# Optimization experiments

Hardware: AMD Instinct MI355X
Metric: run time of the kernel (lower is better)

Reference implementation:

```python
import jax, jax.numpy as jnp
import numpy as np

B, S, D = 4, 4096, 1024   # batch, seq_len, d_model
E, K, H = 8, 2, 2048      # num_experts, top_k, expert hidden dim


def setup_inputs() -> dict:
    key = jax.random.key(0)
    k0, k1, k2, k3, k4 = jax.random.split(key, 5)
    scale = 0.02
    return {
        "x": jax.random.normal(k0, (B, S, D), jnp.float32),
        "gate_w": jax.random.normal(k1, (D, E), jnp.float32) * scale,      # nn.Linear(d_model, E, bias=False)
        "w_gate": jax.random.normal(k2, (E, D, H), jnp.float32) * scale,   # expert SwiGLU gate proj
        "w_up":   jax.random.normal(k3, (E, D, H), jnp.float32) * scale,   # expert up proj
        "w_down": jax.random.normal(k4, (E, H, D), jnp.float32) * scale,   # expert down proj
    }


def reference(x, gate_w, w_gate, w_up, w_down):
    b, s, d = x.shape
    e = gate_w.shape[1]
    x_flat = x.reshape(-1, d)                          # [T, D], T = B*S

    gate_logits = x_flat @ gate_w                      # [T, E] (eval mode: no noise)
    top_logits, top_idx = jax.lax.top_k(gate_logits, K)  # [T, K]
    top_w = jax.nn.softmax(top_logits.astype(jnp.float32), axis=1).astype(x.dtype)  # [T, K]

    # load-balancing aux loss (Switch/Mixtral style)
    f_i = jax.nn.one_hot(top_idx, e, dtype=jnp.float32).sum(axis=1).mean(axis=0)  # [E]
    p_i = jax.nn.softmax(gate_logits, axis=1).mean(axis=0)                        # [E]
    aux_loss = (f_i * p_i).sum() * (e ** 2)

    flat_idx = top_idx.reshape(-1)                     # [T*K] expert ids
    # pre-scale token copies by routing weight (matches original)
    y = (x_flat[:, None, :] * top_w[:, :, None]).reshape(-1, d)  # [T*K, D]

    expert_out = jnp.zeros_like(y)
    for i in range(e):  # fixed small expert count: dense-fallback masked MLP
        h = jax.nn.silu(y @ w_gate[i]) * (y @ w_up[i])           # [T*K, H]
        o_i = h @ w_down[i]                                      # [T*K, D]
        expert_out = jnp.where((flat_idx == i)[:, None], o_i, expert_out)

    # faithful to original: scatter_add indexed by EXPERT id (as written in source)
    final = jnp.zeros_like(x_flat).at[flat_idx].add(expert_out)  # [T, D]
    return final.reshape(b, s, d), aux_loss
```

## Files before the change

kernel.cpp:

```cpp
#include <hip/hip_runtime.h>
#include <hip/hip_bf16.h>
#include <stdint.h>

#define T_TOK  16384
#define DMODEL 1024
#define NEXP   8
#define HDIM   2048
#define CAPSL  16512

#define BM 128
#define BN 128
#define NWORK_MAX 264
#define YROWS_MAX (NWORK_MAX*BM)
#define GRID_GEMM (NWORK_MAX * 16)

#define OFF_COUNTS 0
#define OFF_NWORK  64
#define OFF_FSUM   128
#define OFF_PSUM   192
#define OFF_WORK   256
#define OFF_HSUM   8192
#define OFF_ZERO_END 73728
#define OFF_TOK    131072
#define OFF_WGT    786432
#define OFF_WT     2097152
#define WT_ELEMS   (NEXP*HDIM*DMODEL)
#define OFF_Y      (OFF_WT + (size_t)2*WT_ELEMS*2)
#define NEED_FAST  (OFF_Y + (size_t)YROWS_MAX*DMODEL*2)

typedef __attribute__((ext_vector_type(4))) float f32x4;
typedef __attribute__((ext_vector_type(8))) short bf16x8;

__device__ __forceinline__ unsigned short f2bf(float f) {
    unsigned int u = __builtin_bit_cast(unsigned int, f);
    unsigned int r = (u + 0x7fffu + ((u >> 16) & 1u)) >> 16;
    return (unsigned short)r;
}

__global__ __launch_bounds__(256) void wt_fragment(const float* __restrict__ wg,
                                                   const float* __restrict__ wu,
                                                   unsigned short* __restrict__ wt_out) {
    int mat = blockIdx.z;
    const float* src = mat ? wu : wg;
    unsigned short* dst = wt_out + (size_t)mat * WT_ELEMS;
    int e  = blockIdx.y;
    int kt = blockIdx.x & 15;
    int ht = blockIdx.x >> 4;
    __shared__ unsigned short tile[64][68];
    const float* s = src + ((size_t)e * DMODEL + kt * 64) * HDIM + ht * 64;
    for (int u = threadIdx.x; u < 1024; u += 256) {
        int r = u >> 4, c = (u & 15) * 4;
        float4 v = *(const float4*)(s + (size_t)r * HDIM + c);
        tile[r][c + 0] = f2bf(v.x); tile[r][c + 1] = f2bf(v.y);
        tile[r][c + 2] = f2bf(v.z); tile[r][c + 3] = f2bf(v.w);
    }
    __syncthreads();
    for (int cc = threadIdx.x; cc < 512; cc += 256) {
        int r   = cc & 15;
        int q   = (cc >> 4) & 3;
        int sl  = (cc >> 6) & 1;
        int ntl = cc >> 7;
        int hh  = ntl * 16 + r;
        int ddb = sl * 32 + q * 8;
        bf16x8 o;
        #pragma unroll
        for (int j = 0; j < 8; ++j) o[j] = (short)tile[ddb + j][hh];
        size_t idx = ((((size_t)e * 128 + ht * 4 + ntl) * 32 + kt * 2 + sl) * 4 + q) * 128
                     + r * 8;
        *(bf16x8*)(dst + idx) = o;
    }
}

__global__ __launch_bounds__(256) void gating(const float* __restrict__ x,
                                              const float* __restrict__ gw,
                                              int* counts, float* fsum, float* psum,
                                              int* tok_list, float* wgt_list) {
    __shared__ float gws_t[NEXP * DMODEL];
    __shared__ int   ch_e[64][2];
    __shared__ float ch_w[64][2];
    __shared__ float pacc[NEXP];
    __shared__ int   hist[NEXP], gbase[NEXP], cursor[NEXP];
    if (threadIdx.x < NEXP) { pacc[threadIdx.x] = 0.f; hist[threadIdx.x] = 0; cursor[threadIdx.x] = 0; }
    for (int u = threadIdx.x; u < NEXP * DMODEL; u += 256) {
        gws_t[(u & 7) * DMODEL + (u >> 3)] = gw[u];
    }
    __syncthreads();
    int wave = threadIdx.x >> 6, lane = threadIdx.x & 63;
    int tbase = blockIdx.x * 64;
    for (int it = 0; it < 16; ++it) {
        int slot = wave * 16 + it;
        int t = tbase + slot;
        float p[8] = {0, 0, 0, 0, 0, 0, 0, 0};
        #pragma unroll
        for (int j = 0; j < 16; ++j) {
            float xv = x[(size_t)t * DMODEL + j * 64 + lane];
            #pragma unroll
            for (int e2 = 0; e2 < 8; ++e2) p[e2] += xv * gws_t[e2 * DMODEL + j * 64 + lane];
        }
        #pragma unroll
        for (int off = 32; off >= 1; off >>= 1) {
            #pragma unroll
            for (int e2 = 0; e2 < 8; ++e2) p[e2] += __shfl_xor(p[e2], off);
        }
        if (lane == 0) {
            int i0 = 0; float l0 = p[0];
            #pragma unroll
            for (int e2 = 1; e2 < 8; ++e2) if (p[e2] > l0) { l0 = p[e2]; i0 = e2; }
            int i1 = -1; float l1 = -1e30f;
            #pragma unroll
            for (int e2 = 0; e2 < 8; ++e2) if (e2 != i0 && p[e2] > l1) { l1 = p[e2]; i1 = e2; }
            float a = __expf(l1 - l0);
            float w0 = 1.f / (1.f + a);
            ch_e[slot][0] = i0; ch_e[slot][1] = i1;
            ch_w[slot][0] = w0; ch_w[slot][1] = a * w0;
            atomicAdd(&hist[i0], 1); atomicAdd(&hist[i1], 1);
            float s = 0.f, ex[8];
            #pragma unroll
            for (int e2 = 0; e2 < 8; ++e2) { ex[e2] = __expf(p[e2] - l0); s += ex[e2]; }
            float inv = 1.f / s;
            #pragma unroll
            for (int e2 = 0; e2 < 8; ++e2) atomicAdd(&pacc[e2], ex[e2] * inv);
        }
    }
    __syncthreads();
    if (threadIdx.x < NEXP) {
        int h = hist[threadIdx.x];
        gbase[threadIdx.x] = atomicAdd(&counts[threadIdx.x], h);
        atomicAdd(&fsum[threadIdx.x], (float)h);
        atomicAdd(&psum[threadIdx.x], pacc[threadIdx.x]);
    }
    __syncthreads();
    if (threadIdx.x < 64) {
        int slot = threadIdx.x, t = tbase + slot;
        #pragma unroll
        for (int k2 = 0; k2 < 2; ++k2) {
            int e2 = ch_e[slot][k2];
            int pos = gbase[e2] + atomicAdd(&cursor[e2], 1);
            tok_list[e2 * CAPSL + pos] = t;
            wgt_list[e2 * CAPSL + pos] = ch_w[slot][k2];
        }
    }
}

__global__ void build_work(const int* counts, int4* work, int* n_work,
                           const float* fsum, const float* psum, float* out_aux) {
    int lane = threadIdx.x;
    if (lane < NEXP) {
        int base_t = 0;
        for (int j = 0; j < lane; ++j) base_t += (counts[j] + BM - 1) / BM;
        int nt = (counts[lane] + BM - 1) / BM;
        for (int r = 0; r < nt; ++r)
            work[base_t + r] = make_int4(lane, r * BM, (base_t + r) * BM, 0);
        if (lane == NEXP - 1) *n_work = base_t + nt;
    }
    if (lane == 0) {
        float aux = 0.f;
        for (int e = 0; e < NEXP; ++e)
            aux += (fsum[e] / (float)T_TOK) * (psum[e] / (float)T_TOK);
        *out_aux = aux * (float)(NEXP * NEXP);
    }
}

__global__ __launch_bounds__(256) void materialize(const float* __restrict__ x,
                                                   const int* __restrict__ tok_list,
                                                   const float* __restrict__ wgt_list,
                                                   const int* __restrict__ counts,
                                                   const int4* __restrict__ work,
                                                   const int* __restrict__ n_work,
                                                   unsigned short* __restrict__ yfrag) {
    int w = blockIdx.x; if (w >= *n_work) return;
    int4 wi = work[w];
    int e = wi.x, row0 = wi.y, yb = wi.z;
    int cnt = counts[e];
    int rtb  = (yb >> 4) + blockIdx.y * 4;
    int rloc = blockIdx.y * 64;
    for (int v = threadIdx.x; v < 8192; v += 256) {
        int r   = v & 15;
        int q   = (v >> 4) & 3;
        int s   = (v >> 6) & 31;
        int rtl = v >> 11;
        int slot = row0 + rloc + rtl * 16 + r;
        bf16x8 o;
        if (slot < cnt) {
            int t = tok_list[e * CAPSL + slot];
            float wgt = wgt_list[e * CAPSL + slot];
            const float* xp = x + (size_t)t * DMODEL + s * 32 + q * 8;
            float4 v0 = *(const float4*)xp;
            float4 v1 = *(const float4*)(xp + 4);
            o[0] = f2bf(v0.x * wgt); o[1] = f2bf(v0.y * wgt);
            o[2] = f2bf(v0.z * wgt); o[3] = f2bf(v0.w * wgt);
            o[4] = f2bf(v1.x * wgt); o[5] = f2bf(v1.y * wgt);
            o[6] = f2bf(v1.z * wgt); o[7] = f2bf(v1.w * wgt);
        } else {
            #pragma unroll
            for (int j = 0; j < 8; ++j) o[j] = 0;
        }
        *(bf16x8*)(yfrag + (size_t)(rtb + rtl) * 16384 + (s * 4 + q) * 128 + r * 8) = o;
    }
}

#define MMG(AF, GF) do {                                                               \
    __builtin_amdgcn_s_setprio(1);                                                     \
    _Pragma("unroll")                                                                  \
    for (int mi = 0; mi < 4; ++mi) {                                                   \
        _Pragma("unroll")                                                              \
        for (int ni = 0; ni < 4; ++ni)                                                 \
            accg[mi][ni] = __builtin_amdgcn_mfma_f32_16x16x32_bf16(AF[mi], GF[ni], accg[mi][ni], 0, 0, 0); \
    }                                                                                  \
    __builtin_amdgcn_s_setprio(0);                                                     \
} while (0)

#define MMU(AF, UF) do {                                                               \
    __builtin_amdgcn_s_setprio(1);                                                     \
    _Pragma("unroll")                                                                  \
    for (int mi = 0; mi < 4; ++mi) {                                                   \
        _Pragma("unroll")                                                              \
        for (int ni = 0; ni < 4; ++ni)                                                 \
            accu[mi][ni] = __builtin_amdgcn_mfma_f32_16x16x32_bf16(AF[mi], UF[ni], accu[mi][ni], 0, 0, 0); \
    }                                                                                  \
    __builtin_amdgcn_s_setprio(0);                                                     \
} while (0)

#define LD_AG(ASET, GSET, o_) do {                                                     \
    _Pragma("unroll")                                                                  \
    for (int mi = 0; mi < 4; ++mi) ASET[mi] = pA[mi][o_];                              \
    _Pragma("unroll")                                                                  \
    for (int ni = 0; ni < 4; ++ni) GSET[ni] = pG[ni][o_];                              \
    __builtin_amdgcn_sched_barrier(0);                                                 \
} while (0)

#define LD_U(USET, o_) do {                                                            \
    _Pragma("unroll")                                                                  \
    for (int ni = 0; ni < 4; ++ni) USET[ni] = pU[ni][o_];                              \
    __builtin_amdgcn_sched_barrier(0);                                                 \
} while (0)

__global__ __launch_bounds__(256, 2) void moe_gemm_fast(
        const unsigned short* __restrict__ yfrag,
        const unsigned short* __restrict__ wfrag,
        const int4* __restrict__ work, const int* __restrict__ n_work,
        float* __restrict__ hsum) {
    __shared__ float red[4][64];
    int bid = blockIdx.x;
    int xcd = bid & 7, idx = bid >> 3;
    int w  = xcd * 33 + (idx >> 4);
    int nb = idx & 15;
    if (w >= *n_work) return;
    int4 wi = work[w];
    int e = wi.x, yb = wi.z;
    int tid = threadIdx.x, wave = tid >> 6, lane = tid & 63;
    int wm = wave >> 1, wn = wave & 1;

    const bf16x8* pA[4]; const bf16x8* pG[4]; const bf16x8* pU[4];
    #pragma unroll
    for (int mi = 0; mi < 4; ++mi)
        pA[mi] = (const bf16x8*)(yfrag + (size_t)((yb >> 4) + wm * 4 + mi) * 16384 + lane * 8);
    #pragma unroll
    for (int ni = 0; ni < 4; ++ni) {
        size_t nt = (size_t)e * 128 + nb * 8 + wn * 4 + ni;
        pG[ni] = (const bf16x8*)(wfrag + nt * 16384 + lane * 8);
        pU[ni] = (const bf16x8*)(wfrag + (size_t)WT_ELEMS + nt * 16384 + lane * 8);
    }

    f32x4 accg[4][4], accu[4][4];
    #pragma unroll
    for (int mi = 0; mi < 4; ++mi)
        #pragma unroll
        for (int ni = 0; ni < 4; ++ni) {
            accg[mi][ni] = (f32x4){0.f, 0.f, 0.f, 0.f};
            accu[mi][ni] = (f32x4){0.f, 0.f, 0.f, 0.f};
        }

    bf16x8 aA[4], gA[4], uA[4], aB[4], gB[4], uB[4];

    LD_AG(aA, gA, 0);
    LD_U(uA, 0);

    #pragma unroll 1
    for (int s = 0; s < 30; s += 2) {
        int o1 = (s + 1) * 64, o2 = (s + 2) * 64;
        LD_AG(aB, gB, o1);
        MMG(aA, gA);
        LD_U(uB, o1);
        MMU(aA, uA);
        LD_AG(aA, gA, o2);
        MMG(aB, gB);
        LD_U(uA, o2);
        MMU(aB, uB);
    }
    LD_AG(aB, gB, 31 * 64);
    MMG(aA, gA);
    LD_U(uB, 31 * 64);
    MMU(aA, uA);
    MMG(aB, gB);
    MMU(aB, uB);

    #pragma unroll
    for (int ni = 0; ni < 4; ++ni) {
        float s = 0.f;
        #pragma unroll
        for (int mi = 0; mi < 4; ++mi)
            #pragma unroll
            for (int i = 0; i < 4; ++i) {
                float gv = accg[mi][ni][i], uv = accu[mi][ni][i];
                s += (gv / (1.f + __expf(-gv))) * uv;
            }
        s += __shfl_xor(s, 16);
        s += __shfl_xor(s, 32);
        if (lane < 16) red[wave][ni * 16 + lane] = s;
    }
    __syncthreads();
    if (tid < BN) {
        int wnc = tid >> 6, ix = tid & 63;
        float v = red[wnc][ix] + red[2 + wnc][ix];
        atomicAdd(&hsum[(size_t)e * HDIM + nb * 128 + tid], v);
    }
}

__global__ __launch_bounds__(256) void moe_slow(const float* __restrict__ x,
                                                const int* __restrict__ tok_list,
                                                const float* __restrict__ wgt_list,
                                                const int* __restrict__ counts,
                                                const float* __restrict__ wgate,
                                                const float* __restrict__ wup,
                                                float* __restrict__ hsum) {
    int e = blockIdx.x;
    int h = blockIdx.y * 256 + threadIdx.x;
    int cnt = counts[e];
    __shared__ float xs[DMODEL];
    float acc = 0.f;
    for (int i = 0; i < cnt; ++i) {
        int t = tok_list[e * CAPSL + i];
        float wv = wgt_list[e * CAPSL + i];
        for (int u = threadIdx.x; u < DMODEL; u += 256)
            xs[u] = x[(size_t)t * DMODEL + u] * wv;
        __syncthreads();
        float g = 0.f, uvv = 0.f;
        for (int k = 0; k < DMODEL; ++k) {
            float xv = xs[k];
            g   += xv * wgate[((size_t)e * DMODEL + k) * HDIM + h];
            uvv += xv * wup[((size_t)e * DMODEL + k) * HDIM + h];
        }
        acc += (g / (1.f + __expf(-g))) * uvv;
        __syncthreads();
    }
    atomicAdd(&hsum[(size_t)e * HDIM + h], acc);
}

__global__ __launch_bounds__(256) void down_proj(const float* __restrict__ hsum,
                                                 const float* __restrict__ wd,
                                                 float* __restrict__ out) {
    int e    = blockIdx.x;
    int dblk = blockIdx.y;
    int hblk = blockIdx.z;
    __shared__ float sh[256];
    int h0 = hblk * 256;
    sh[threadIdx.x] = hsum[(size_t)e * HDIM + h0 + threadIdx.x];
    __syncthreads();
    int d = dblk * 256 + threadIdx.x;
    const float* wp = wd + ((size_t)e * HDIM + h0) * DMODEL + d;
    float acc = 0.f;
    #pragma unroll 4
    for (int h = 0; h < 256; h += 4) {
        float4 s4 = *(const float4*)&sh[h];
        acc += s4.x * wp[(size_t)(h + 0) * DMODEL];
        acc += s4.y * wp[(size_t)(h + 1) * DMODEL];
        acc += s4.z * wp[(size_t)(h + 2) * DMODEL];
        acc += s4.w * wp[(size_t)(h + 3) * DMODEL];
    }
    atomicAdd(&out[(size_t)e * DMODEL + d], acc);
}

extern "C" void kernel_launch(void* const* d_in, const int* in_sizes, int n_in,
                              void* d_out, int out_size, void* d_ws, size_t ws_size,
                              hipStream_t stream) {
    const float* x     = (const float*)d_in[0];
    const float* gw    = (const float*)d_in[1];
    const float* wgate = (const float*)d_in[2];
    const float* wup   = (const float*)d_in[3];
    const float* wdown = (const float*)d_in[4];
    float* out = (float*)d_out;
    char*  ws  = (char*)d_ws;

    int*   counts = (int*)(ws + OFF_COUNTS);
    int*   nwork  = (int*)(ws + OFF_NWORK);
    float* fsum   = (float*)(ws + OFF_FSUM);
    float* psum   = (float*)(ws + OFF_PSUM);
    int4*  workv  = (int4*)(ws + OFF_WORK);
    float* hsum   = (float*)(ws + OFF_HSUM);
    int*   tok    = (int*)(ws + OFF_TOK);
    float* wgt    = (float*)(ws + OFF_WGT);
    unsigned short* wt   = (unsigned short*)(ws + OFF_WT);
    unsigned short* ybuf = (unsigned short*)(ws + OFF_Y);

    hipMemsetAsync(d_out, 0, (size_t)out_size * sizeof(float), stream);
    hipMemsetAsync(d_ws, 0, OFF_ZERO_END, stream);

    gating<<<256, 256, 0, stream>>>(x, gw, counts, fsum, psum, tok, wgt);
    build_work<<<1, 64, 0, stream>>>(counts, workv, nwork, fsum, psum,
                                     out + (size_t)T_TOK * DMODEL);

    bool fast = ws_size >= NEED_FAST;
    if (fast) {
        wt_fragment<<<dim3(512, 8, 2), 256, 0, stream>>>(wgate, wup, wt);
        materialize<<<dim3(NWORK_MAX, 2), 256, 0, stream>>>(x, tok, wgt, counts, workv, nwork, ybuf);
        moe_gemm_fast<<<dim3(GRID_GEMM), 256, 0, stream>>>(ybuf, wt, workv, nwork, hsum);
    } else {
        moe_slow<<<dim3(NEXP, HDIM / 256), 256, 0, stream>>>(x, tok, wgt, counts,
                                                             wgate, wup, hsum);
    }

    down_proj<<<dim3(NEXP, 4, 8), 256, 0, stream>>>(hsum, wdown, out);
}
```

Baseline: 451.9 us.

## Stage MoE GEMM operands through LDS with async global-to-LDS loads and 256-row tiles

The fused gate/up expert GEMM now uses 512-thread blocks with a 256-row M tile. Operand fragments are staged into a 4-slot LDS ring buffer through global_load_lds, three slices ahead, so the A and weight fragments are shared across waves. Each wave no longer loads its operands directly from global memory into registers. This cuts redundant global/L2 traffic and doubles weight reuse per row tile. In exchange it adds block barriers, 128KB of dynamic LDS with one block per CU, and more padding waste from the larger tiles and the changed work-list sizing.

Result: faster. 424.2 us (-6.1%).

```diff
diff --git a/kernel.cpp b/kernel.cpp
--- a/kernel.cpp
+++ b/kernel.cpp
@@ -8,10 +8,11 @@
 #define HDIM   2048
 #define CAPSL  16512
 
-#define BM 128
+#define BM 256
 #define BN 128
-#define NWORK_MAX 264
+#define NWORK_MAX 136
 #define YROWS_MAX (NWORK_MAX*BM)
+#define SLOT_BYTES 32768
 #define GRID_GEMM (NWORK_MAX * 16)
 
 #define OFF_COUNTS 0
@@ -35,6 +36,11 @@
     unsigned int u = __builtin_bit_cast(unsigned int, f);
     unsigned int r = (u + 0x7fffu + ((u >> 16) & 1u)) >> 16;
     return (unsigned short)r;
+}
+
+__device__ __forceinline__ void glds16(const void* g, void* l) {
+    __builtin_amdgcn_global_load_lds((const __attribute__((address_space(1))) void*)g,
+                                     (__attribute__((address_space(3))) void*)l, 16, 0, 0);
 }
 
 __global__ __launch_bounds__(256) void wt_fragment(const float* __restrict__ wg,
@@ -199,68 +205,92 @@
     }
 }
 
-#define MMG(AF, GF) do {                                                               \
+#define SLICE(h_, DO_STAGE, VM_) do {                                                  \
+    const char* sp = smem + ((h_) & 3) * SLOT_BYTES;                                   \
+    bf16x8 af[4], bg[4], bu[4];                                                        \
+    _Pragma("unroll")                                                                  \
+    for (int mi = 0; mi < 4; ++mi)                                                     \
+        af[mi] = *(const bf16x8*)(sp + (wm * 4 + mi) * 1024 + lane * 16);              \
+    _Pragma("unroll")                                                                  \
+    for (int ni = 0; ni < 4; ++ni)                                                     \
+        bg[ni] = *(const bf16x8*)(sp + (16 + wn * 4 + ni) * 1024 + lane * 16);         \
+    if (DO_STAGE) {                                                                    \
+        int k3 = ((h_) + 3) * 512;                                                     \
+        char* sb = smem + (((h_) + 3) & 3) * SLOT_BYTES;                               \
+        glds16(gsrc0 + k3, sb + dst0);                                                 \
+        glds16(gsrc1 + k3, sb + dst1);                                                 \
+    }                                                                                  \
+    asm volatile("s_waitcnt lgkmcnt(0)" ::: "memory");                                 \
+    __builtin_amdgcn_sched_barrier(0);                                                 \
     __builtin_amdgcn_s_setprio(1);                                                     \
     _Pragma("unroll")                                                                  \
-    for (int mi = 0; mi < 4; ++mi) {                                                   \
+    for (int mi = 0; mi < 4; ++mi)                                                     \
         _Pragma("unroll")                                                              \
         for (int ni = 0; ni < 4; ++ni)                                                 \
-            accg[mi][ni] = __builtin_amdgcn_mfma_f32_16x16x32_bf16(AF[mi], GF[ni], accg[mi][ni], 0, 0, 0); \
+            accg[mi][ni] = __builtin_amdgcn_mfma_f32_16x16x32_bf16(af[mi], bg[ni], accg[mi][ni], 0, 0, 0); \
+    __builtin_amdgcn_s_setprio(0);                                                     \
+    _Pragma("unroll")                                                                  \
+    for (int ni = 0; ni < 4; ++ni)                                                     \
+        bu[ni] = *(const bf16x8*)(sp + (24 + wn * 4 + ni) * 1024 + lane * 16);         \
+    if (DO_STAGE) {                                                                    \
+        int k3 = ((h_) + 3) * 512;                                                     \
+        char* sb = smem + (((h_) + 3) & 3) * SLOT_BYTES;                               \
+        glds16(gsrc2 + k3, sb + dst2);                                                 \
+        glds16(gsrc3 + k3, sb + dst3);                                                 \
     }                                                                                  \
-    __builtin_amdgcn_s_setprio(0);                                                     \
-} while (0)
-
-#define MMU(AF, UF) do {                                                               \
+    asm volatile("s_waitcnt lgkmcnt(0)" ::: "memory");                                 \
+    __builtin_amdgcn_sched_barrier(0);                                                 \
     __builtin_amdgcn_s_setprio(1);                                                     \
     _Pragma("unroll")                                                                  \
-    for (int mi = 0; mi < 4; ++mi) {                                                   \
+    for (int mi = 0; mi < 4; ++mi)                                                     \
         _Pragma("unroll")                                                              \
         for (int ni = 0; ni < 4; ++ni)                                                 \
-            accu[mi][ni] = __builtin_amdgcn_mfma_f32_16x16x32_bf16(AF[mi], UF[ni], accu[mi][ni], 0, 0, 0); \
-    }                                                                                  \
+            accu[mi][ni] = __builtin_amdgcn_mfma_f32_16x16x32_bf16(af[mi], bu[ni], accu[mi][ni], 0, 0, 0); \
     __builtin_amdgcn_s_setprio(0);                                                     \
+    __builtin_amdgcn_sched_barrier(0);                                                 \
+    if ((VM_) == 8)      asm volatile("s_waitcnt vmcnt(8)" ::: "memory");              \
+    else if ((VM_) == 4) asm volatile("s_waitcnt vmcnt(4)" ::: "memory");              \
+    else if ((VM_) == 0) asm volatile("s_waitcnt vmcnt(0)" ::: "memory");              \
+    if ((VM_) >= 0) __builtin_amdgcn_s_barrier();                                      \
 } while (0)
 
-#define LD_AG(ASET, GSET, o_) do {                                                     \
-    _Pragma("unroll")                                                                  \
-    for (int mi = 0; mi < 4; ++mi) ASET[mi] = pA[mi][o_];                              \
-    _Pragma("unroll")                                                                  \
-    for (int ni = 0; ni < 4; ++ni) GSET[ni] = pG[ni][o_];                              \
-    __builtin_amdgcn_sched_barrier(0);                                                 \
-} while (0)
-
-#define LD_U(USET, o_) do {                                                            \
-    _Pragma("unroll")                                                                  \
-    for (int ni = 0; ni < 4; ++ni) USET[ni] = pU[ni][o_];                              \
-    __builtin_amdgcn_sched_barrier(0);                                                 \
-} while (0)
-
-__global__ __launch_bounds__(256, 2) void moe_gemm_fast(
+__global__ __launch_bounds__(512, 1) void moe_gemm_fast(
         const unsigned short* __restrict__ yfrag,
         const unsigned short* __restrict__ wfrag,
         const int4* __restrict__ work, const int* __restrict__ n_work,
         float* __restrict__ hsum) {
-    __shared__ float red[4][64];
+    extern __shared__ char smem[];
+    __shared__ float red[8][64];
     int bid = blockIdx.x;
     int xcd = bid & 7, idx = bid >> 3;
-    int w  = xcd * 33 + (idx >> 4);
-    int nb = idx & 15;
+    int nbc = idx / 68;
+    int rem = idx - nbc * 68;
+    int w   = xcd * 17 + (rem >> 2);
+    int nb  = nbc * 4 + (rem & 3);
     if (w >= *n_work) return;
     int4 wi = work[w];
     int e = wi.x, yb = wi.z;
     int tid = threadIdx.x, wave = tid >> 6, lane = tid & 63;
     int wm = wave >> 1, wn = wave & 1;
 
-    const bf16x8* pA[4]; const bf16x8* pG[4]; const bf16x8* pU[4];
+    int c0 = wave * 4;
+    int rt0 = yb >> 4;
+    const unsigned short* gs[4]; int dsb[4];
     #pragma unroll
-    for (int mi = 0; mi < 4; ++mi)
-        pA[mi] = (const bf16x8*)(yfrag + (size_t)((yb >> 4) + wm * 4 + mi) * 16384 + lane * 8);
-    #pragma unroll
-    for (int ni = 0; ni < 4; ++ni) {
-        size_t nt = (size_t)e * 128 + nb * 8 + wn * 4 + ni;
-        pG[ni] = (const bf16x8*)(wfrag + nt * 16384 + lane * 8);
-        pU[ni] = (const bf16x8*)(wfrag + (size_t)WT_ELEMS + nt * 16384 + lane * 8);
-    }
+    for (int i = 0; i < 4; ++i) {
+        int c = c0 + i;
+        const unsigned short* base;
+        if (c < 16)       base = yfrag + (size_t)(rt0 + c) * 16384;
+        else if (c < 24)  base = wfrag + ((size_t)e * 128 + nb * 8 + (c - 16)) * 16384;
+        else              base = wfrag + (size_t)WT_ELEMS
+                                 + ((size_t)e * 128 + nb * 8 + (c - 24)) * 16384;
+        gs[i]  = base + lane * 8;
+        dsb[i] = c * 1024;
+    }
+    const unsigned short* gsrc0 = gs[0]; int dst0 = dsb[0];
+    const unsigned short* gsrc1 = gs[1]; int dst1 = dsb[1];
+    const unsigned short* gsrc2 = gs[2]; int dst2 = dsb[2];
+    const unsigned short* gsrc3 = gs[3]; int dst3 = dsb[3];
 
     f32x4 accg[4][4], accu[4][4];
     #pragma unroll
@@ -271,29 +301,25 @@
             accu[mi][ni] = (f32x4){0.f, 0.f, 0.f, 0.f};
         }
 
-    bf16x8 aA[4], gA[4], uA[4], aB[4], gB[4], uB[4];
-
-    LD_AG(aA, gA, 0);
-    LD_U(uA, 0);
+    #pragma unroll
+    for (int h = 0; h < 3; ++h) {
+        char* sb = smem + h * SLOT_BYTES;
+        int k0 = h * 512;
+        glds16(gsrc0 + k0, sb + dst0);
+        glds16(gsrc1 + k0, sb + dst1);
+        glds16(gsrc2 + k0, sb + dst2);
+        glds16(gsrc3 + k0, sb + dst3);
+    }
+    asm volatile("s_waitcnt vmcnt(8)" ::: "memory");
+    __builtin_amdgcn_s_barrier();
 
     #pragma unroll 1
-    for (int s = 0; s < 30; s += 2) {
-        int o1 = (s + 1) * 64, o2 = (s + 2) * 64;
-        LD_AG(aB, gB, o1);
-        MMG(aA, gA);
-        LD_U(uB, o1);
-        MMU(aA, uA);
-        LD_AG(aA, gA, o2);
-        MMG(aB, gB);
-        LD_U(uA, o2);
-        MMU(aB, uB);
-    }
-    LD_AG(aB, gB, 31 * 64);
-    MMG(aA, gA);
-    LD_U(uB, 31 * 64);
-    MMU(aA, uA);
-    MMG(aB, gB);
-    MMU(aB, uB);
+    for (int h = 0; h < 29; ++h) {
+        SLICE(h, true, 8);
+    }
+    SLICE(29, false, 4);
+    SLICE(30, false, 0);
+    SLICE(31, false, -1);
 
     #pragma unroll
     for (int ni = 0; ni < 4; ++ni) {
@@ -312,7 +338,7 @@
     __syncthreads();
     if (tid < BN) {
         int wnc = tid >> 6, ix = tid & 63;
-        float v = red[wnc][ix] + red[2 + wnc][ix];
+        float v = red[wnc][ix] + red[2 + wnc][ix] + red[4 + wnc][ix] + red[6 + wnc][ix];
         atomicAdd(&hsum[(size_t)e * HDIM + nb * 128 + tid], v);
     }
 }
@@ -393,6 +419,9 @@
     unsigned short* wt   = (unsigned short*)(ws + OFF_WT);
     unsigned short* ybuf = (unsigned short*)(ws + OFF_Y);
 
+    hipFuncSetAttribute(reinterpret_cast<const void*>(moe_gemm_fast),
+                        hipFuncAttributeMaxDynamicSharedMemorySize, 4 * SLOT_BYTES);
+
     hipMemsetAsync(d_out, 0, (size_t)out_size * sizeof(float), stream);
     hipMemsetAsync(d_ws, 0, OFF_ZERO_END, stream);
 
@@ -403,8 +432,9 @@
     bool fast = ws_size >= NEED_FAST;
     if (fast) {
         wt_fragment<<<dim3(512, 8, 2), 256, 0, stream>>>(wgate, wup, wt);
-        materialize<<<dim3(NWORK_MAX, 2), 256, 0, stream>>>(x, tok, wgt, counts, workv, nwork, ybuf);
-        moe_gemm_fast<<<dim3(GRID_GEMM), 256, 0, stream>>>(ybuf, wt, workv, nwork, hsum);
+        materialize<<<dim3(NWORK_MAX, 4), 256, 0, stream>>>(x, tok, wgt, counts, workv, nwork, ybuf);
+        moe_gemm_fast<<<dim3(GRID_GEMM), 512, 4 * SLOT_BYTES, stream>>>(
+            ybuf, wt, workv, nwork, hsum);
     } else {
         moe_slow<<<dim3(NEXP, HDIM / 256), 256, 0, stream>>>(x, tok, wgt, counts,
                                                              wgate, wup, hsum);
```
